# Kernel tuning notes

Measured on AMD Instinct MI355X. Metric: run time of the kernel, lower is better.

Reference implementation:

```python
import jax, jax.numpy as jnp
import numpy as np

N_NODES = 100000
IN_C, HID_C, OUT_C = 128, 64, 5
NEG_SLOPE = 0.01  # F.leaky_relu default


def gcn_conv(x, W, b, src_sl, dst_sl, norm, n_nodes):
    """PyG GCNConv: h = D^{-1/2}(A+I)D^{-1/2} (x W) + b.
    src_sl/dst_sl already include self-loops; norm is the per-edge coefficient."""
    h = x @ W                              # [N, out]
    msg = h[src_sl] * norm[:, None]        # [E+N, out] gather + scale
    agg = jax.ops.segment_sum(msg, dst_sl, num_segments=n_nodes)
    return agg + b


def setup_inputs() -> dict:
    key = jax.random.key(0)
    ks = jax.random.split(key, 8)
    n, e = N_NODES, 1600000
    x = jax.random.normal(ks[0], (n, IN_C), dtype=jnp.float32)
    edge_index = jax.random.randint(ks[1], (2, e), 0, n, dtype=jnp.int64)
    idx = jax.random.randint(ks[2], (20000,), 0, n, dtype=jnp.int64)
    # Glorot-ish init for GCNConv weights, kaiming-ish for MLP
    W0 = jax.random.normal(ks[3], (IN_C, HID_C), dtype=jnp.float32) * (1.0 / np.sqrt(IN_C))
    b0 = jnp.zeros((HID_C,), dtype=jnp.float32)
    W1 = jax.random.normal(ks[4], (HID_C, HID_C), dtype=jnp.float32) * (1.0 / np.sqrt(HID_C))
    b1 = jnp.zeros((HID_C,), dtype=jnp.float32)
    Wm = jax.random.normal(ks[5], (HID_C, OUT_C), dtype=jnp.float32) * (1.0 / np.sqrt(HID_C))
    bm = jnp.zeros((OUT_C,), dtype=jnp.float32)
    return {"x": x, "edge_index": edge_index, "idx": idx,
            "W0": W0, "b0": b0, "W1": W1, "b1": b1, "Wm": Wm, "bm": bm}


def reference(x, edge_index, idx, W0, b0, W1, b1, Wm, bm):
    n = x.shape[0]
    src, dst = edge_index[0], edge_index[1]
    loops = jnp.arange(n, dtype=edge_index.dtype)
    src_sl = jnp.concatenate([src, loops])
    dst_sl = jnp.concatenate([dst, loops])
    # symmetric normalization with self-loops (gcn_norm)
    deg = jax.ops.segment_sum(jnp.ones_like(dst_sl, dtype=x.dtype), dst_sl, num_segments=n)
    dinv = jnp.where(deg > 0, jax.lax.rsqrt(deg), 0.0)
    norm = dinv[src_sl] * dinv[dst_sl]     # [E+N]

    h = jax.nn.leaky_relu(gcn_conv(x, W0, b0, src_sl, dst_sl, norm, n), NEG_SLOPE)
    h = jax.nn.leaky_relu(gcn_conv(h, W1, b1, src_sl, dst_sl, norm, n), NEG_SLOPE)

    h_sel = h[idx]                          # index_select on node dim
    out = jax.nn.sigmoid(h_sel @ Wm + bm)
    return (h_sel, out)
```

## Files before the change

### kernel.cpp

```cpp
#include <hip/hip_runtime.h>
#include <hip/hip_fp16.h>
#include <math.h>


#define NPART 64
#define MAXB 2048

typedef _Float16 h8 __attribute__((ext_vector_type(8)));
typedef float f4v __attribute__((ext_vector_type(4)));

__device__ __forceinline__ float lrelu(float x) { return x > 0.0f ? x : 0.01f * x; }


__global__ __launch_bounds__(1024) void k_part_hist(const int* __restrict__ dst, int E,
                                                    int B, int* __restrict__ phist) {
    __shared__ int scnt[MAXB];
    int t = threadIdx.x, p = blockIdx.x;
    for (int i = t; i < B; i += 1024) scnt[i] = 0;
    __syncthreads();
    int ep = (((E + NPART - 1) / NPART) + 3) & ~3;
    int beg = p * ep, endi = min(E, beg + ep);
    int cnt4 = (endi - beg) >> 2;
    for (int i = t; i < cnt4; i += 1024) {
        int4 d = *(const int4*)(dst + beg + i * 4);
        atomicAdd(&scnt[d.x >> 6], 1);
        atomicAdd(&scnt[d.y >> 6], 1);
        atomicAdd(&scnt[d.z >> 6], 1);
        atomicAdd(&scnt[d.w >> 6], 1);
    }
    int rem = (endi - beg) & 3;
    if (t < rem) atomicAdd(&scnt[dst[beg + cnt4 * 4 + t] >> 6], 1);
    __syncthreads();
    for (int i = t; i < B; i += 1024) phist[i * NPART + p] = scnt[i];
}

__global__ __launch_bounds__(1024) void k_part_scatter(const int* __restrict__ src,
                                                       const int* __restrict__ dst, int E,
                                                       int B, const int* __restrict__ pbase,
                                                       int* __restrict__ esA) {
    __shared__ int sbase[MAXB];
    int t = threadIdx.x, p = blockIdx.x;
    for (int i = t; i < B; i += 1024) sbase[i] = pbase[i * NPART + p];
    __syncthreads();
    int ep = (((E + NPART - 1) / NPART) + 3) & ~3;
    int beg = p * ep, endi = min(E, beg + ep);
    int cnt4 = (endi - beg) >> 2;
    for (int i = t; i < cnt4; i += 1024) {
        int e = beg + i * 4;
        int4 d = *(const int4*)(dst + e);
        int4 s = *(const int4*)(src + e);
        int p0 = atomicAdd(&sbase[d.x >> 6], 1);
        int p1 = atomicAdd(&sbase[d.y >> 6], 1);
        int p2 = atomicAdd(&sbase[d.z >> 6], 1);
        int p3 = atomicAdd(&sbase[d.w >> 6], 1);
        esA[p0] = ((d.x & 63) << 24) | s.x;
        esA[p1] = ((d.y & 63) << 24) | s.y;
        esA[p2] = ((d.z & 63) << 24) | s.z;
        esA[p3] = ((d.w & 63) << 24) | s.w;
    }
    int rem = (endi - beg) & 3;
    if (t < rem) {
        int e = beg + cnt4 * 4 + t;
        int d = dst[e];
        int pos = atomicAdd(&sbase[d >> 6], 1);
        esA[pos] = ((d & 63) << 24) | src[e];
    }
}


__global__ void k_blocksum(const int* __restrict__ cnt, int N, int* __restrict__ bsum) {
    __shared__ int sm[256];
    int b = blockIdx.x, t = threadIdx.x;
    int base = b * 1024 + t * 4;
    int s = 0;
#pragma unroll
    for (int i = 0; i < 4; ++i) { int j = base + i; if (j < N) s += cnt[j]; }
    sm[t] = s; __syncthreads();
    for (int off = 128; off > 0; off >>= 1) {
        if (t < off) sm[t] += sm[t + off];
        __syncthreads();
    }
    if (t == 0) bsum[b] = sm[0];
}

__global__ void k_scan_bsum(int* __restrict__ bsum, int nb, int* __restrict__ offN) {
    __shared__ int sm[1024];
    int t = threadIdx.x;
    int v = (t < nb) ? bsum[t] : 0;
    sm[t] = v; __syncthreads();
    for (int d = 1; d < 1024; d <<= 1) {
        int add = (t >= d) ? sm[t - d] : 0;
        __syncthreads();
        sm[t] += add;
        __syncthreads();
    }
    if (t < nb) bsum[t] = sm[t] - v;
    if (t == nb - 1) *offN = sm[t];
}

__global__ void k_scan_block(const int* __restrict__ cnt, const int* __restrict__ bsum,
                             int* __restrict__ off, int N) {
    __shared__ int sm[256];
    int b = blockIdx.x, t = threadIdx.x;
    int base = b * 1024 + t * 4;
    int v[4];
#pragma unroll
    for (int i = 0; i < 4; ++i) { int j = base + i; v[i] = (j < N) ? cnt[j] : 0; }
    int tsum = v[0] + v[1] + v[2] + v[3];
    sm[t] = tsum; __syncthreads();
    for (int d = 1; d < 256; d <<= 1) {
        int val = (t >= d) ? sm[t - d] : 0;
        __syncthreads();
        sm[t] += val;
        __syncthreads();
    }
    int run = sm[t] - tsum + bsum[b];
#pragma unroll
    for (int i = 0; i < 4; ++i) {
        int j = base + i;
        if (j < N) off[j] = run;
        run += v[i];
    }
}


__global__ __launch_bounds__(256) void k_bsort(const int* __restrict__ pbase, int BP,
                                               const int* __restrict__ esA,
                                               int* __restrict__ esB,
                                               int* __restrict__ off,
                                               float* __restrict__ dinv,
                                               int N, int E) {
    __shared__ int hcnt[64];
    __shared__ int hoff[64];
    int t = threadIdx.x, b = blockIdx.x;
    int start = pbase[b * NPART];
    int endi  = pbase[min((b + 1) * NPART, BP)];
    int cnt = endi - start;

    if (t < 64) hcnt[t] = 0;
    __syncthreads();
    for (int i = t * 4; i < cnt; i += 1024) {
#pragma unroll
        for (int c = 0; c < 4; ++c)
            if (i + c < cnt) atomicAdd(&hcnt[(esA[start + i + c] >> 24) & 63], 1);
    }
    __syncthreads();

    if (t < 64) {
        int c = hcnt[t];
        int v = c;
#pragma unroll
        for (int d = 1; d < 64; d <<= 1) {
            int u = __shfl_up(v, d);
            if (t >= d) v += u;
        }
        int pos = start + (v - c);
        hoff[t] = pos;
        int g = b * 64 + t;
        if (g < N) {
            off[g] = pos;
            dinv[g] = rsqrtf((float)c + 1.0f);
        }
        if (g == N - 1) off[N] = E;
    }
    __syncthreads();
    if (t < 64) hcnt[t] = hoff[t];
    __syncthreads();

    for (int i = t * 4; i < cnt; i += 1024) {
#pragma unroll
        for (int c = 0; c < 4; ++c)
            if (i + c < cnt) {
                int v = esA[start + i + c];
                int pos = atomicAdd(&hcnt[(v >> 24) & 63], 1);
                esB[pos] = v & 0xFFFFFF;
            }
    }
}


template <int K>
__global__ __launch_bounds__(256) void k_gemm(const float* __restrict__ A,
                                              const float* __restrict__ W,
                                              const float* __restrict__ dinv,
                                              __half* __restrict__ hout, int N) {
    constexpr int ASTR = K + 8;
    __shared__ _Float16 a16[64 * ASTR];
    __shared__ _Float16 wt16[64 * ASTR];
    int t = threadIdx.x, lane = t & 63, wv = t >> 6;
    int rowBase = blockIdx.x * 64;

#pragma unroll
    for (int i = 0; i < K / 16; ++i) {
        int g = i * 256 + t;
        int r = g / (K / 4), kq = g % (K / 4);
        int gr = rowBase + r; if (gr >= N) gr = N - 1;
        float4 v = *(const float4*)(A + (size_t)gr * K + kq * 4);
        _Float16* p = a16 + r * ASTR + kq * 4;
        *(__half2*)(p)     = __floats2half2_rn(v.x, v.y);
        *(__half2*)(p + 2) = __floats2half2_rn(v.z, v.w);
    }
#pragma unroll
    for (int i = 0; i < K / 16; ++i) {
        int g = i * 256 + t;
        int k = g >> 4, nq = g & 15;
        float4 v = *(const float4*)(W + (size_t)k * 64 + nq * 4);
        wt16[(nq * 4 + 0) * ASTR + k] = (_Float16)v.x;
        wt16[(nq * 4 + 1) * ASTR + k] = (_Float16)v.y;
        wt16[(nq * 4 + 2) * ASTR + k] = (_Float16)v.z;
        wt16[(nq * 4 + 3) * ASTR + k] = (_Float16)v.w;
    }
    __syncthreads();

    int m = lane & 15, q = lane >> 4;
    f4v acc[4] = {{0,0,0,0},{0,0,0,0},{0,0,0,0},{0,0,0,0}};
    const _Float16* arow = a16 + (wv * 16 + m) * ASTR + q * 8;
#pragma unroll
    for (int kt = 0; kt < K / 32; ++kt) {
        h8 af = *(const h8*)(arow + kt * 32);
#pragma unroll
        for (int nt = 0; nt < 4; ++nt) {
            h8 bf = *(const h8*)(wt16 + (nt * 16 + m) * ASTR + kt * 32 + q * 8);
            acc[nt] = __builtin_amdgcn_mfma_f32_16x16x32_f16(af, bf, acc[nt], 0, 0, 0);
        }
    }

    int r0 = rowBase + wv * 16 + q * 4;
#pragma unroll
    for (int reg = 0; reg < 4; ++reg) {
        int row = r0 + reg;
        if (row >= N) continue;
        float dv = dinv[row];
#pragma unroll
        for (int nt = 0; nt < 4; ++nt)
            hout[(size_t)row * 64 + nt * 16 + m] = (__half)(acc[nt][reg] * dv);
    }
}


template <bool APPLY>
__global__ __launch_bounds__(256) void k_agg(const int* __restrict__ off,
                                             const int* __restrict__ esB,
                                             const float* __restrict__ dinv,
                                             const __half* __restrict__ hs,
                                             const float* __restrict__ b0,
                                             float* __restrict__ agg, int N) {
    int lane = threadIdx.x & 63;
    int node = (blockIdx.x * blockDim.x + threadIdx.x) >> 6;
    if (node >= N) return;
    int qt = lane >> 4, l16 = lane & 15;
    int beg = off[node], end = off[node + 1];

    float ax = 0, ay = 0, az = 0, aw = 0;
    auto addrow = [&](int s) {
        uint2 u = *(const uint2*)(hs + (size_t)s * 64 + l16 * 4);
        float2 f0 = __half22float2(*(__half2*)&u.x);
        float2 f1 = __half22float2(*(__half2*)&u.y);
        ax += f0.x; ay += f0.y; az += f1.x; aw += f1.y;
    };
    if (qt == 0) addrow(node);
    int j = beg + qt;
    for (; j + 4 < end; j += 8) { addrow(esB[j]); addrow(esB[j + 4]); }
    if (j < end) addrow(esB[j]);

#pragma unroll
    for (int d = 16; d <= 32; d <<= 1) {
        ax += __shfl_xor(ax, d); ay += __shfl_xor(ay, d);
        az += __shfl_xor(az, d); aw += __shfl_xor(aw, d);
    }
    if (qt == 0) {
        float dv = dinv[node];
        float4 o; o.x = ax * dv; o.y = ay * dv; o.z = az * dv; o.w = aw * dv;
        if (APPLY) {
            float4 b = *(const float4*)(b0 + l16 * 4);
            o.x = lrelu(o.x + b.x); o.y = lrelu(o.y + b.y);
            o.z = lrelu(o.z + b.z); o.w = lrelu(o.w + b.w);
        }
        *(float4*)(agg + (size_t)node * 64 + l16 * 4) = o;
    }
}


__global__ void k_out(const int* __restrict__ idx, const float* __restrict__ agg,
                      const float* __restrict__ b1, const float* __restrict__ Wm,
                      const float* __restrict__ bm, float* __restrict__ out, int NSEL) {
    int lane = threadIdx.x & 63;
    int wv = (blockIdx.x * blockDim.x + threadIdx.x) >> 6;
    if (wv >= NSEL) return;
    int node = idx[wv];
    float hs = lrelu(agg[(size_t)node * 64 + lane] + b1[lane]);
    out[(size_t)wv * 64 + lane] = hs;
#pragma unroll
    for (int o = 0; o < 5; ++o) {
        float p = hs * Wm[lane * 5 + o];
#pragma unroll
        for (int offs = 32; offs > 0; offs >>= 1) p += __shfl_down(p, offs);
        if (lane == 0)
            out[(size_t)NSEL * 64 + (size_t)wv * 5 + o] =
                1.0f / (1.0f + expf(-(p + bm[o])));
    }
}

extern "C" void kernel_launch(void* const* d_in, const int* in_sizes, int n_in,
                              void* d_out, int out_size, void* d_ws, size_t ws_size,
                              hipStream_t stream) {
    const float* x   = (const float*)d_in[0];
    const int*   ei  = (const int*)d_in[1];
    const int*   idx = (const int*)d_in[2];
    const float* W0  = (const float*)d_in[3];
    const float* b0  = (const float*)d_in[4];
    const float* W1  = (const float*)d_in[5];
    const float* b1  = (const float*)d_in[6];
    const float* Wm  = (const float*)d_in[7];
    const float* bm  = (const float*)d_in[8];

    int N    = in_sizes[0] / 128;
    int E    = in_sizes[1] / 2;
    int NSEL = in_sizes[2];
    const int* src = ei;
    const int* dst = ei + E;

    int B  = (N + 63) / 64;
    int BP = B * NPART;

    char* w = (char*)d_ws;
    size_t Na  = ((size_t)N + 1023) & ~(size_t)1023;
    size_t Ea  = ((size_t)E + 1023) & ~(size_t)1023;
    size_t BPa = ((size_t)BP + 1023) & ~(size_t)1023;
    float*  dinv  = (float*)w;                w += Na * 4;
    int*    phist = (int*)w;                  w += BPa * 4;
    int*    pbase = (int*)w;                  w += (BPa + 1024) * 4;
    int*    bsum  = (int*)w;                  w += 1024 * 4;
    int*    off   = (int*)w;                  w += (Na + 1024) * 4;
    int*    esA   = (int*)w;                  w += Ea * 4;
    int*    esB   = (int*)w;                  w += Ea * 4;
    __half* hs16  = (__half*)w;               w += (size_t)N * 64 * 2;
    float*  agg   = (float*)w;

    int nbp = (BP + 1023) / 1024;

    k_part_hist<<<NPART, 1024, 0, stream>>>(dst, E, B, phist);
    k_blocksum<<<nbp, 256, 0, stream>>>(phist, BP, bsum);
    k_scan_bsum<<<1, 1024, 0, stream>>>(bsum, nbp, pbase + BP);
    k_scan_block<<<nbp, 256, 0, stream>>>(phist, bsum, pbase, BP);
    k_part_scatter<<<NPART, 1024, 0, stream>>>(src, dst, E, B, pbase, esA);
    k_bsort<<<B, 256, 0, stream>>>(pbase, BP, esA, esB, off, dinv, N, E);

    int gemm_blocks = (N + 63) / 64;
    int agg_blocks  = (N + 3) / 4;

    k_gemm<128><<<gemm_blocks, 256, 0, stream>>>(x, W0, dinv, hs16, N);
    k_agg<true><<<agg_blocks, 256, 0, stream>>>(off, esB, dinv, hs16, b0, agg, N);
    k_gemm<64><<<gemm_blocks, 256, 0, stream>>>(agg, W1, dinv, hs16, N);
    k_agg<false><<<agg_blocks, 256, 0, stream>>>(off, esB, dinv, hs16, nullptr, agg, N);
    k_out<<<(NSEL + 3) / 4, 256, 0, stream>>>(idx, agg, b1, Wm, bm, (float*)d_out, NSEL);
}
```

Before: 277.6 us.

## Aggregate second GCN layer only for selected nodes and fuse with output MLP

The second aggregation now runs only for the 20000 selected nodes, fused with the bias, leaky-relu and the output linear-plus-sigmoid head, so aggregation of all 100000 nodes and the separate output kernel are skipped. The first aggregation writes fp16 output, which the second GEMM reads directly, halving that intermediate's traffic. The gather loops are unrolled to issue four independent row loads per iteration for more memory-level parallelism. Storing the layer-1 activations in fp16 adds some rounding error.

```diff
diff --git a/kernel.cpp b/kernel.cpp
--- a/kernel.cpp
+++ b/kernel.cpp
@@ -179,8 +179,8 @@
 }
 
 
-template <int K>
-__global__ __launch_bounds__(256) void k_gemm(const float* __restrict__ A,
+template <int K, typename AT>
+__global__ __launch_bounds__(256) void k_gemm(const AT* __restrict__ A,
                                               const float* __restrict__ W,
                                               const float* __restrict__ dinv,
                                               __half* __restrict__ hout, int N) {
@@ -195,10 +195,14 @@
         int g = i * 256 + t;
         int r = g / (K / 4), kq = g % (K / 4);
         int gr = rowBase + r; if (gr >= N) gr = N - 1;
-        float4 v = *(const float4*)(A + (size_t)gr * K + kq * 4);
         _Float16* p = a16 + r * ASTR + kq * 4;
-        *(__half2*)(p)     = __floats2half2_rn(v.x, v.y);
-        *(__half2*)(p + 2) = __floats2half2_rn(v.z, v.w);
+        if constexpr (sizeof(AT) == 4) {
+            float4 v = *(const float4*)((const float*)A + (size_t)gr * K + kq * 4);
+            *(__half2*)(p)     = __floats2half2_rn(v.x, v.y);
+            *(__half2*)(p + 2) = __floats2half2_rn(v.z, v.w);
+        } else {
+            *(uint2*)p = *(const uint2*)((const __half*)A + (size_t)gr * K + kq * 4);
+        }
     }
 #pragma unroll
     for (int i = 0; i < K / 16; ++i) {
@@ -238,13 +242,12 @@
 }
 
 
-template <bool APPLY>
-__global__ __launch_bounds__(256) void k_agg(const int* __restrict__ off,
-                                             const int* __restrict__ esB,
-                                             const float* __restrict__ dinv,
-                                             const __half* __restrict__ hs,
-                                             const float* __restrict__ b0,
-                                             float* __restrict__ agg, int N) {
+__global__ __launch_bounds__(256) void k_agg1(const int* __restrict__ off,
+                                              const int* __restrict__ esB,
+                                              const float* __restrict__ dinv,
+                                              const __half* __restrict__ hs,
+                                              const float* __restrict__ b0,
+                                              __half* __restrict__ aout, int N) {
     int lane = threadIdx.x & 63;
     int node = (blockIdx.x * blockDim.x + threadIdx.x) >> 6;
     if (node >= N) return;
@@ -252,16 +255,20 @@
     int beg = off[node], end = off[node + 1];
 
     float ax = 0, ay = 0, az = 0, aw = 0;
-    auto addrow = [&](int s) {
-        uint2 u = *(const uint2*)(hs + (size_t)s * 64 + l16 * 4);
+    auto ld = [&](int s) { return *(const uint2*)(hs + (size_t)s * 64 + l16 * 4); };
+    auto acc4 = [&](uint2 u) {
         float2 f0 = __half22float2(*(__half2*)&u.x);
         float2 f1 = __half22float2(*(__half2*)&u.y);
         ax += f0.x; ay += f0.y; az += f1.x; aw += f1.y;
     };
-    if (qt == 0) addrow(node);
+    if (qt == 0) acc4(ld(node));
     int j = beg + qt;
-    for (; j + 4 < end; j += 8) { addrow(esB[j]); addrow(esB[j + 4]); }
-    if (j < end) addrow(esB[j]);
+    for (; j + 12 < end; j += 16) {
+        int s0 = esB[j], s1 = esB[j + 4], s2 = esB[j + 8], s3 = esB[j + 12];
+        uint2 u0 = ld(s0), u1 = ld(s1), u2 = ld(s2), u3 = ld(s3);
+        acc4(u0); acc4(u1); acc4(u2); acc4(u3);
+    }
+    for (; j < end; j += 4) acc4(ld(esB[j]));
 
 #pragma unroll
     for (int d = 16; d <= 32; d <<= 1) {
@@ -270,31 +277,69 @@
     }
     if (qt == 0) {
         float dv = dinv[node];
-        float4 o; o.x = ax * dv; o.y = ay * dv; o.z = az * dv; o.w = aw * dv;
-        if (APPLY) {
-            float4 b = *(const float4*)(b0 + l16 * 4);
-            o.x = lrelu(o.x + b.x); o.y = lrelu(o.y + b.y);
-            o.z = lrelu(o.z + b.z); o.w = lrelu(o.w + b.w);
-        }
-        *(float4*)(agg + (size_t)node * 64 + l16 * 4) = o;
-    }
-}
-
-
-__global__ void k_out(const int* __restrict__ idx, const float* __restrict__ agg,
-                      const float* __restrict__ b1, const float* __restrict__ Wm,
-                      const float* __restrict__ bm, float* __restrict__ out, int NSEL) {
+        float4 b = *(const float4*)(b0 + l16 * 4);
+        float ox = lrelu(ax * dv + b.x), oy = lrelu(ay * dv + b.y);
+        float oz = lrelu(az * dv + b.z), ow = lrelu(aw * dv + b.w);
+        uint2 u;
+        *(__half2*)&u.x = __floats2half2_rn(ox, oy);
+        *(__half2*)&u.y = __floats2half2_rn(oz, ow);
+        *(uint2*)(aout + (size_t)node * 64 + l16 * 4) = u;
+    }
+}
+
+
+__global__ __launch_bounds__(256) void k_aggout(const int* __restrict__ idx,
+                                                const int* __restrict__ off,
+                                                const int* __restrict__ esB,
+                                                const float* __restrict__ dinv,
+                                                const __half* __restrict__ hs,
+                                                const float* __restrict__ b1,
+                                                const float* __restrict__ Wm,
+                                                const float* __restrict__ bm,
+                                                float* __restrict__ out, int NSEL) {
     int lane = threadIdx.x & 63;
     int wv = (blockIdx.x * blockDim.x + threadIdx.x) >> 6;
     if (wv >= NSEL) return;
     int node = idx[wv];
-    float hs = lrelu(agg[(size_t)node * 64 + lane] + b1[lane]);
-    out[(size_t)wv * 64 + lane] = hs;
+    int qt = lane >> 4, l16 = lane & 15;
+    int beg = off[node], end = off[node + 1];
+
+    float ax = 0, ay = 0, az = 0, aw = 0;
+    auto ld = [&](int s) { return *(const uint2*)(hs + (size_t)s * 64 + l16 * 4); };
+    auto acc4 = [&](uint2 u) {
+        float2 f0 = __half22float2(*(__half2*)&u.x);
+        float2 f1 = __half22float2(*(__half2*)&u.y);
+        ax += f0.x; ay += f0.y; az += f1.x; aw += f1.y;
+    };
+    if (qt == 0) acc4(ld(node));
+    int j = beg + qt;
+    for (; j + 12 < end; j += 16) {
+        int s0 = esB[j], s1 = esB[j + 4], s2 = esB[j + 8], s3 = esB[j + 12];
+        uint2 u0 = ld(s0), u1 = ld(s1), u2 = ld(s2), u3 = ld(s3);
+        acc4(u0); acc4(u1); acc4(u2); acc4(u3);
+    }
+    for (; j < end; j += 4) acc4(ld(esB[j]));
+
+#pragma unroll
+    for (int d = 16; d <= 32; d <<= 1) {
+        ax += __shfl_xor(ax, d); ay += __shfl_xor(ay, d);
+        az += __shfl_xor(az, d); aw += __shfl_xor(aw, d);
+    }
+
+    float dv = dinv[node];
+    float4 b = *(const float4*)(b1 + l16 * 4);
+    float4 hsel;
+    hsel.x = lrelu(ax * dv + b.x); hsel.y = lrelu(ay * dv + b.y);
+    hsel.z = lrelu(az * dv + b.z); hsel.w = lrelu(aw * dv + b.w);
+    if (qt == 0) *(float4*)(out + (size_t)wv * 64 + l16 * 4) = hsel;
+
+    const float* wr = Wm + (size_t)(4 * l16) * 5;
 #pragma unroll
     for (int o = 0; o < 5; ++o) {
-        float p = hs * Wm[lane * 5 + o];
-#pragma unroll
-        for (int offs = 32; offs > 0; offs >>= 1) p += __shfl_down(p, offs);
+        float p = hsel.x * wr[o] + hsel.y * wr[5 + o] +
+                  hsel.z * wr[10 + o] + hsel.w * wr[15 + o];
+        p += __shfl_xor(p, 1); p += __shfl_xor(p, 2);
+        p += __shfl_xor(p, 4); p += __shfl_xor(p, 8);
         if (lane == 0)
             out[(size_t)NSEL * 64 + (size_t)wv * 5 + o] =
                 1.0f / (1.0f + expf(-(p + bm[o])));
@@ -335,7 +380,7 @@
     int*    esA   = (int*)w;                  w += Ea * 4;
     int*    esB   = (int*)w;                  w += Ea * 4;
     __half* hs16  = (__half*)w;               w += (size_t)N * 64 * 2;
-    float*  agg   = (float*)w;
+    __half* a16g  = (__half*)w;
 
     int nbp = (BP + 1023) / 1024;
 
@@ -349,9 +394,9 @@
     int gemm_blocks = (N + 63) / 64;
     int agg_blocks  = (N + 3) / 4;
 
-    k_gemm<128><<<gemm_blocks, 256, 0, stream>>>(x, W0, dinv, hs16, N);
-    k_agg<true><<<agg_blocks, 256, 0, stream>>>(off, esB, dinv, hs16, b0, agg, N);
-    k_gemm<64><<<gemm_blocks, 256, 0, stream>>>(agg, W1, dinv, hs16, N);
-    k_agg<false><<<agg_blocks, 256, 0, stream>>>(off, esB, dinv, hs16, nullptr, agg, N);
-    k_out<<<(NSEL + 3) / 4, 256, 0, stream>>>(idx, agg, b1, Wm, bm, (float*)d_out, NSEL);
-}
+    k_gemm<128, float><<<gemm_blocks, 256, 0, stream>>>(x, W0, dinv, hs16, N);
+    k_agg1<<<agg_blocks, 256, 0, stream>>>(off, esB, dinv, hs16, b0, a16g, N);
+    k_gemm<64, __half><<<gemm_blocks, 256, 0, stream>>>(a16g, W1, dinv, hs16, N);
+    k_aggout<<<(NSEL + 3) / 4, 256, 0, stream>>>(idx, off, esB, dinv, hs16, b1, Wm, bm,
+                                                 (float*)d_out, NSEL);
+}
```

Result: faster. 259.2 us (-6.6%).
